# Kernel tuning notes

Measured on AMD Instinct MI355X. Metric: run time of the kernel, lower is better.

## Reference

```python
import jax, jax.numpy as jnp
import numpy as np
import math

RES = 1024
HEADS = 16
HEAD_RES = RES // HEADS
B, S = 2, 2048


def setup_inputs() -> dict:
    key = jax.random.key(0)
    kx, kq, kk, kv = jax.random.split(key, 4)
    scale = 1.0 / math.sqrt(RES)
    return {
        "x": jax.random.normal(kx, (B, S, RES), dtype=jnp.float32),
        "Wq": jax.random.normal(kq, (RES, RES), dtype=jnp.float32) * scale,
        "Wk": jax.random.normal(kk, (RES, RES), dtype=jnp.float32) * scale,
        "Wv": jax.random.normal(kv, (RES, RES), dtype=jnp.float32) * scale,
    }


def reference(x, Wq, Wk, Wv):
    batch, seq, _ = x.shape
    # projections (torch Linear without bias: x @ W.T; here W stored as [in, out])
    def split_heads(t):
        return t.reshape(batch, seq, HEADS, HEAD_RES).transpose(0, 2, 1, 3)  # [B,H,S,D]
    q = split_heads(x @ Wq)
    k = split_heads(x @ Wk)
    v = split_heads(x @ Wv)
    scores = jnp.einsum("bhsd,bhtd->bhst", q, k) / math.sqrt(HEAD_RES)
    attn = jax.nn.softmax(scores, axis=-1)
    out = jnp.einsum("bhst,bhtd->bhsd", attn, v)  # [B,H,S,D]
    return out.transpose(0, 2, 1, 3).reshape(batch, seq, RES)
```

## Files before the change

### kernel.cpp

```cpp
#include <hip/hip_runtime.h>

typedef _Float16 f16;
typedef _Float16 half8 __attribute__((ext_vector_type(8)));
typedef float f32x4 __attribute__((ext_vector_type(4)));
typedef unsigned int u32x4 __attribute__((ext_vector_type(4)));

#define RES 1024
#define NH 16
#define HD 64
#define BATCH 2
#define SEQ 2048
#define M_ROWS (BATCH * SEQ)

__device__ __forceinline__ void gload_lds16(const void* g, void* l) {
  __builtin_amdgcn_global_load_lds(
      (const __attribute__((address_space(1))) unsigned int*)g,
      (__attribute__((address_space(3))) unsigned int*)l, 16, 0, 0);
}

__device__ __forceinline__ unsigned pk16(float a, float b) {
  auto h = __builtin_amdgcn_cvt_pkrtz(a, b);
  return __builtin_bit_cast(unsigned, h);
}

__device__ __forceinline__ unsigned pk16_rne(float a, float b) {
  unsigned short la = __builtin_bit_cast(unsigned short, (f16)a);
  unsigned short hb = __builtin_bit_cast(unsigned short, (f16)b);
  return (unsigned)la | ((unsigned)hb << 16);
}

__device__ __forceinline__ void swap32(unsigned a, unsigned b, unsigned& x, unsigned& y) {
#if __has_builtin(__builtin_amdgcn_permlane32_swap)
  auto t = __builtin_amdgcn_permlane32_swap(a, b, false, false);
  x = (unsigned)t[0];
  y = (unsigned)t[1];
#else
  unsigned ax = __shfl_xor(a, 32), bx = __shfl_xor(b, 32);
  int hi = (threadIdx.x & 63) >> 5;
  x = hi ? bx : a;
  y = hi ? b : ax;
#endif
}

__device__ __forceinline__ void swap16(unsigned a, unsigned b, unsigned& x, unsigned& y) {
#if __has_builtin(__builtin_amdgcn_permlane16_swap)
  auto t = __builtin_amdgcn_permlane16_swap(a, b, false, false);
  x = (unsigned)t[0];
  y = (unsigned)t[1];
#else
  unsigned ax = __shfl_xor(a, 16), bx = __shfl_xor(b, 16);
  int q1 = ((threadIdx.x & 63) >> 4) & 1;
  x = q1 ? bx : a;
  y = q1 ? b : ax;
#endif
}

__global__ __launch_bounds__(256) void prep_kernel(const float* __restrict__ x,
                                                   const float* __restrict__ Wq,
                                                   const float* __restrict__ Wk,
                                                   const float* __restrict__ Wv,
                                                   f16* __restrict__ xh,
                                                   f16* __restrict__ Wt) {
  __shared__ float tile[32][33];
  int bid = blockIdx.x;
  int tid = threadIdx.x;
  if (bid < 2048) {
    int idx = bid * 256 + tid;
    const float4* xv = (const float4*)x;
    float4 a = xv[idx * 2];
    float4 b = xv[idx * 2 + 1];
    half8 h;
    h[0] = (f16)a.x; h[1] = (f16)a.y; h[2] = (f16)a.z; h[3] = (f16)a.w;
    h[4] = (f16)b.x; h[5] = (f16)b.y; h[6] = (f16)b.z; h[7] = (f16)b.w;
    ((half8*)xh)[idx] = h;
  } else {
    int wb = bid - 2048;
    int bz = wb >> 10;
    int rem = wb & 1023;
    int by = rem >> 5, bx = rem & 31;
    const float* W = bz == 0 ? Wq : (bz == 1 ? Wk : Wv);
    f16* Wo = Wt + (size_t)bz * RES * RES;
    int tx = tid & 31, ty = tid >> 5;
#pragma unroll
    for (int i = 0; i < 4; i++)
      tile[ty + i * 8][tx] = W[(size_t)(by * 32 + ty + i * 8) * RES + bx * 32 + tx];
    __syncthreads();
#pragma unroll
    for (int i = 0; i < 4; i++)
      Wo[(size_t)(bx * 32 + ty + i * 8) * RES + by * 32 + tx] = (f16)tile[tx][ty + i * 8];
  }
}

__global__ __launch_bounds__(256) void proj_gemm_kernel(const f16* __restrict__ xh,
                                                        const f16* __restrict__ Wt,
                                                        f16* __restrict__ Qh,
                                                        f16* __restrict__ Kh,
                                                        f16* __restrict__ Vt) {
  int proj = blockIdx.z;
  const f16* Bt = Wt + (size_t)proj * RES * RES;
  int m0 = blockIdx.x * 128;
  int n0 = blockIdx.y * 128;
  __shared__ alignas(16) f16 Als[128 * 32];
  __shared__ alignas(16) f16 Bls[128 * 32];
  int t = threadIdx.x, lane = t & 63, w = t >> 6;
  int l15 = lane & 15, quad = lane >> 4;
  int wm = w >> 1, wn = w & 1;

  f32x4 zero = {0.f, 0.f, 0.f, 0.f};
  f32x4 acc[4][4];
#pragma unroll
  for (int mt = 0; mt < 4; mt++)
#pragma unroll
    for (int nt = 0; nt < 4; nt++) acc[mt][nt] = zero;

  for (int k0 = 0; k0 < RES; k0 += 32) {
#pragma unroll
    for (int i = 0; i < 2; i++) {
      int wl = i * 256 + w * 64;
      int linear = wl + lane;
      int row = linear >> 2;
      int kk = (linear & 3) * 8;
      gload_lds16(xh + (size_t)(m0 + row) * RES + k0 + kk, &Als[wl * 8]);
      gload_lds16(Bt + (size_t)(n0 + row) * RES + k0 + kk, &Bls[wl * 8]);
    }
    __syncthreads();
    half8 af[4], bf[4];
#pragma unroll
    for (int mt = 0; mt < 4; mt++)
      af[mt] = *(const half8*)&Als[(wm * 64 + mt * 16 + l15) * 32 + quad * 8];
#pragma unroll
    for (int nt = 0; nt < 4; nt++)
      bf[nt] = *(const half8*)&Bls[(wn * 64 + nt * 16 + l15) * 32 + quad * 8];
#pragma unroll
    for (int mt = 0; mt < 4; mt++)
#pragma unroll
      for (int nt = 0; nt < 4; nt++)
        acc[mt][nt] = __builtin_amdgcn_mfma_f32_16x16x32_f16(af[mt], bf[nt], acc[mt][nt], 0, 0, 0);
    __syncthreads();
  }

  if (proj == 2) {
    int rowb = m0 + wm * 64;
    int b = rowb >> 11;
    int sbase = rowb & (SEQ - 1);
    int h = (n0 + wn * 64) >> 6;
    size_t bh = (size_t)b * NH + h;
#pragma unroll
    for (int nt = 0; nt < 4; nt++) {
      unsigned wp[4][2];
#pragma unroll
      for (int mt = 0; mt < 4; mt++) {
        wp[mt][0] = pk16_rne(acc[mt][nt][0], acc[mt][nt][1]);
        wp[mt][1] = pk16_rne(acc[mt][nt][2], acc[mt][nt][3]);
      }
#pragma unroll
      for (int ks = 0; ks < 2; ks++) {
        u32x4 pw;
#pragma unroll
        for (int i = 0; i < 2; i++) {
          unsigned a, bb, xx, yy;
          swap32(wp[2 * ks][i], wp[2 * ks + 1][i], a, bb);
          swap16(a, bb, xx, yy);
          pw[i] = xx;
          pw[2 + i] = yy;
        }
        int d = nt * 16 + l15;
        int s0 = sbase + ks * 32 + quad * 8;
        *(half8*)&Vt[(bh * HD + d) * SEQ + s0] = __builtin_bit_cast(half8, pw);
      }
    }
  } else {
#pragma unroll
    for (int mt = 0; mt < 4; mt++) {
#pragma unroll
      for (int nt = 0; nt < 4; nt++) {
#pragma unroll
        for (int r = 0; r < 4; r++) {
          int row = m0 + wm * 64 + mt * 16 + quad * 4 + r;
          int col = n0 + wn * 64 + nt * 16 + l15;
          f16 v = (f16)acc[mt][nt][r];
          int b = row >> 11, s = row & (SEQ - 1);
          int h = col >> 6, d = col & (HD - 1);
          size_t bh = (size_t)b * NH + h;
          if (proj == 0)
            Qh[(bh * SEQ + s) * HD + d] = v;
          else
            Kh[(bh * SEQ + s) * HD + d] = v;
        }
      }
    }
  }
}

__global__ __launch_bounds__(128, 3) void flash_kernel(const f16* __restrict__ Qh,
                                                       const f16* __restrict__ Kh,
                                                       const f16* __restrict__ Vt,
                                                       float* __restrict__ out) {
  int L = blockIdx.x;
  int xcd = L & 7, slot = L >> 3;
  int bh = ((slot >> 5) << 3) | xcd;
  int qt = slot & 31;
  int b = bh >> 4, h = bh & 15;
  int tid = threadIdx.x;
  int lane = tid & 63, w = tid >> 6;
  int l15 = lane & 15, quad = lane >> 4;
  int qrow0 = qt * 64 + w * 32;

  __shared__ alignas(16) f16 Kls[64 * 64];
  __shared__ alignas(16) f16 Vls[64 * 64];

  const f16* kbase = Kh + (size_t)bh * SEQ * HD;
  const f16* vbase = Vt + (size_t)bh * HD * SEQ;

  int srow = tid >> 3;
  int schunk = tid & 7;

  const f16* qptr = Qh + ((size_t)bh * SEQ + qrow0 + l15) * HD + quad * 8;
  half8 qf[2][2];
  qf[0][0] = *(const half8*)qptr;
  qf[0][1] = *(const half8*)(qptr + 32);
  qf[1][0] = *(const half8*)(qptr + 16 * HD);
  qf[1][1] = *(const half8*)(qptr + 16 * HD + 32);
#pragma unroll
  for (int q2 = 0; q2 < 2; q2++)
#pragma unroll
    for (int ks = 0; ks < 2; ks++)
#pragma unroll
      for (int j = 0; j < 8; j++) qf[q2][ks][j] *= (f16)0.125f;

  f32x4 zero = {0.f, 0.f, 0.f, 0.f};
  float l_acc[2] = {0.f, 0.f};
  f32x4 o[2][4];
#pragma unroll
  for (int q2 = 0; q2 < 2; q2++)
#pragma unroll
    for (int nt = 0; nt < 4; nt++) o[q2][nt] = zero;

  int swz0 = (quad ^ (l15 & 7)) * 8;
  int swz1 = ((quad + 4) ^ (l15 & 7)) * 8;

  auto stage = [&](int kv0) {
#pragma unroll
    for (int rd = 0; rd < 4; rd++) {
      int row = rd * 16 + srow;
      int pc = schunk ^ (row & 7);
      gload_lds16(kbase + ((size_t)(kv0 + row) << 6) + pc * 8,
                  &Kls[rd * 1024 + w * 512]);
      gload_lds16(vbase + ((size_t)row * SEQ) + kv0 + pc * 8,
                  &Vls[rd * 1024 + w * 512]);
    }
  };

  stage(0);

  for (int kv0 = 0; kv0 < SEQ; kv0 += 64) {
    __syncthreads();

    half8 kf0[4], kf1[4];
#pragma unroll
    for (int tt = 0; tt < 4; tt++) {
      int row = tt * 16 + l15;
      kf0[tt] = *(const half8*)&Kls[row * 64 + swz0];
      kf1[tt] = *(const half8*)&Kls[row * 64 + swz1];
    }

    half8 pa[2][2];
#pragma unroll
    for (int q2 = 0; q2 < 2; q2++) {
      f32x4 sc[4];
#pragma unroll
      for (int tt = 0; tt < 4; tt++) {
        sc[tt] = __builtin_amdgcn_mfma_f32_16x16x32_f16(kf0[tt], qf[q2][0], zero, 0, 0, 0);
        sc[tt] = __builtin_amdgcn_mfma_f32_16x16x32_f16(kf1[tt], qf[q2][1], sc[tt], 0, 0, 0);
      }
      float ps = 0.f;
#pragma unroll
      for (int tt = 0; tt < 4; tt++)
#pragma unroll
        for (int r = 0; r < 4; r++) { sc[tt][r] = __expf(sc[tt][r]); ps += sc[tt][r]; }
      ps += __shfl_xor(ps, 16);
      ps += __shfl_xor(ps, 32);
      l_acc[q2] += ps;

      unsigned wp[4][2];
#pragma unroll
      for (int tt = 0; tt < 4; tt++) {
        wp[tt][0] = pk16(sc[tt][0], sc[tt][1]);
        wp[tt][1] = pk16(sc[tt][2], sc[tt][3]);
      }
#pragma unroll
      for (int ks = 0; ks < 2; ks++) {
        u32x4 pw;
#pragma unroll
        for (int i = 0; i < 2; i++) {
          unsigned a, bb, x, y;
          swap32(wp[2 * ks][i], wp[2 * ks + 1][i], a, bb);
          swap16(a, bb, x, y);
          pw[i] = x;
          pw[2 + i] = y;
        }
        pa[q2][ks] = __builtin_bit_cast(half8, pw);
      }
    }

    half8 vf0[4], vf1[4];
#pragma unroll
    for (int nt = 0; nt < 4; nt++) {
      int row = nt * 16 + l15;
      vf0[nt] = *(const half8*)&Vls[row * 64 + swz0];
      vf1[nt] = *(const half8*)&Vls[row * 64 + swz1];
    }

    __syncthreads();

    if (kv0 + 64 < SEQ) stage(kv0 + 64);

#pragma unroll
    for (int q2 = 0; q2 < 2; q2++)
#pragma unroll
      for (int ks = 0; ks < 2; ks++)
#pragma unroll
        for (int nt = 0; nt < 4; nt++)
          o[q2][nt] = __builtin_amdgcn_mfma_f32_16x16x32_f16(pa[q2][ks], ks ? vf1[nt] : vf0[nt], o[q2][nt], 0, 0, 0);
  }

#pragma unroll
  for (int q2 = 0; q2 < 2; q2++) {
    float linv[4];
#pragma unroll
    for (int r = 0; r < 4; r++) linv[r] = 1.0f / __shfl(l_acc[q2], quad * 4 + r);
#pragma unroll
    for (int nt = 0; nt < 4; nt++) {
#pragma unroll
      for (int r = 0; r < 4; r++) {
        int s = qrow0 + q2 * 16 + quad * 4 + r;
        out[((size_t)b * SEQ + s) * RES + h * HD + nt * 16 + l15] = o[q2][nt][r] * linv[r];
      }
    }
  }
}

extern "C" void kernel_launch(void* const* d_in, const int* in_sizes, int n_in,
                              void* d_out, int out_size, void* d_ws, size_t ws_size,
                              hipStream_t stream) {
  (void)in_sizes; (void)n_in; (void)out_size; (void)ws_size;
  const float* x  = (const float*)d_in[0];
  const float* Wq = (const float*)d_in[1];
  const float* Wk = (const float*)d_in[2];
  const float* Wv = (const float*)d_in[3];
  float* out = (float*)d_out;

  f16* xh = (f16*)d_ws;
  f16* Wt = xh + (size_t)M_ROWS * RES;
  f16* Qh = Wt + (size_t)3 * RES * RES;
  f16* Kh = Qh + (size_t)BATCH * NH * SEQ * HD;
  f16* Vt = Kh + (size_t)BATCH * NH * SEQ * HD;

  prep_kernel<<<2048 + 3072, 256, 0, stream>>>(x, Wq, Wk, Wv, xh, Wt);
  proj_gemm_kernel<<<dim3(M_ROWS / 128, RES / 128, 3), 256, 0, stream>>>(xh, Wt, Qh, Kh, Vt);
  flash_kernel<<<1024, 128, 0, stream>>>(Qh, Kh, Vt, out);
}
```

Before: 167.1 us.

## Enlarge projection GEMM tiles to 256x256 with double-buffered swizzled LDS

The QKV projection GEMM now uses 256x256 output tiles with 512 threads, 8x4 MFMA accumulator tiles per wave, and K-steps of 64. LDS is double buffered so the next K slice is fetched with global_load_lds while the current one is computed, using vmcnt waits and raw s_barrier. An XOR swizzle on the LDS layout is meant to cut bank conflicts. The aim is more data reuse per load and overlap of memory with compute. In exchange the grid shrinks to 192 blocks, fewer than the CU count, and register and LDS pressure rise (128 KB of LDS).

```diff
diff --git a/kernel.cpp b/kernel.cpp
--- a/kernel.cpp
+++ b/kernel.cpp
@@ -91,97 +91,125 @@
   }
 }
 
-__global__ __launch_bounds__(256) void proj_gemm_kernel(const f16* __restrict__ xh,
+__global__ __launch_bounds__(512) void proj_gemm_kernel(const f16* __restrict__ xh,
                                                         const f16* __restrict__ Wt,
                                                         f16* __restrict__ Qh,
                                                         f16* __restrict__ Kh,
                                                         f16* __restrict__ Vt) {
   int proj = blockIdx.z;
   const f16* Bt = Wt + (size_t)proj * RES * RES;
-  int m0 = blockIdx.x * 128;
-  int n0 = blockIdx.y * 128;
-  __shared__ alignas(16) f16 Als[128 * 32];
-  __shared__ alignas(16) f16 Bls[128 * 32];
-  int t = threadIdx.x, lane = t & 63, w = t >> 6;
+  int m0 = blockIdx.x * 256;
+  int n0 = blockIdx.y * 256;
+  __shared__ alignas(16) f16 Als[2][256 * 64];
+  __shared__ alignas(16) f16 Bls[2][256 * 64];
+  int tid = threadIdx.x, lane = tid & 63, w = tid >> 6;
   int l15 = lane & 15, quad = lane >> 4;
-  int wm = w >> 1, wn = w & 1;
+  int wr = w >> 2, wc = w & 3;
 
   f32x4 zero = {0.f, 0.f, 0.f, 0.f};
-  f32x4 acc[4][4];
-#pragma unroll
-  for (int mt = 0; mt < 4; mt++)
+  f32x4 acc[8][4];
+#pragma unroll
+  for (int mt = 0; mt < 8; mt++)
 #pragma unroll
     for (int nt = 0; nt < 4; nt++) acc[mt][nt] = zero;
 
-  for (int k0 = 0; k0 < RES; k0 += 32) {
-#pragma unroll
-    for (int i = 0; i < 2; i++) {
-      int wl = i * 256 + w * 64;
-      int linear = wl + lane;
-      int row = linear >> 2;
-      int kk = (linear & 3) * 8;
-      gload_lds16(xh + (size_t)(m0 + row) * RES + k0 + kk, &Als[wl * 8]);
-      gload_lds16(Bt + (size_t)(n0 + row) * RES + k0 + kk, &Bls[wl * 8]);
-    }
-    __syncthreads();
-    half8 af[4], bf[4];
-#pragma unroll
-    for (int mt = 0; mt < 4; mt++)
-      af[mt] = *(const half8*)&Als[(wm * 64 + mt * 16 + l15) * 32 + quad * 8];
-#pragma unroll
-    for (int nt = 0; nt < 4; nt++)
-      bf[nt] = *(const half8*)&Bls[(wn * 64 + nt * 16 + l15) * 32 + quad * 8];
-#pragma unroll
-    for (int mt = 0; mt < 4; mt++)
-#pragma unroll
-      for (int nt = 0; nt < 4; nt++)
-        acc[mt][nt] = __builtin_amdgcn_mfma_f32_16x16x32_f16(af[mt], bf[nt], acc[mt][nt], 0, 0, 0);
-    __syncthreads();
-  }
+  auto stageAB = [&](int k0, int pb) {
+#pragma unroll
+    for (int rnd = 0; rnd < 4; rnd++) {
+      int row = rnd * 64 + (tid >> 3);
+      int pc = (tid & 7) ^ (row & 7);
+      gload_lds16(xh + (size_t)(m0 + row) * RES + k0 + pc * 8,
+                  &Als[pb][rnd * 4096 + w * 512]);
+      gload_lds16(Bt + (size_t)(n0 + row) * RES + k0 + pc * 8,
+                  &Bls[pb][rnd * 4096 + w * 512]);
+    }
+  };
+
+  constexpr int KSTEPS = RES / 64;
+  stageAB(0, 0);
+
+  for (int it = 0; it < KSTEPS; ++it) {
+    int pb = it & 1;
+    if (it + 1 < KSTEPS) {
+      stageAB((it + 1) * 64, pb ^ 1);
+      asm volatile("s_waitcnt vmcnt(8)" ::: "memory");
+    } else {
+      asm volatile("s_waitcnt vmcnt(0)" ::: "memory");
+    }
+    __builtin_amdgcn_sched_barrier(0);
+    __builtin_amdgcn_s_barrier();
+    __builtin_amdgcn_sched_barrier(0);
+
+#pragma unroll
+    for (int half = 0; half < 2; half++) {
+      half8 af[8], bf[4];
+#pragma unroll
+      for (int mt = 0; mt < 8; mt++) {
+        int arow = wr * 128 + mt * 16 + l15;
+        af[mt] = *(const half8*)&Als[pb][arow * 64 + ((half * 4 + quad) ^ (arow & 7)) * 8];
+      }
+#pragma unroll
+      for (int nt = 0; nt < 4; nt++) {
+        int brow = wc * 64 + nt * 16 + l15;
+        bf[nt] = *(const half8*)&Bls[pb][brow * 64 + ((half * 4 + quad) ^ (brow & 7)) * 8];
+      }
+#pragma unroll
+      for (int mt = 0; mt < 8; mt++)
+#pragma unroll
+        for (int nt = 0; nt < 4; nt++)
+          acc[mt][nt] = __builtin_amdgcn_mfma_f32_16x16x32_f16(af[mt], bf[nt], acc[mt][nt], 0, 0, 0);
+    }
+
+    __builtin_amdgcn_sched_barrier(0);
+    __builtin_amdgcn_s_barrier();
+    __builtin_amdgcn_sched_barrier(0);
+  }
+
+  int rowbase = m0 + wr * 128;
+  int b = rowbase >> 11;
+  int sbase = rowbase & (SEQ - 1);
+  int colbase = n0 + wc * 64;
+  int h = colbase >> 6;
+  size_t bh = (size_t)b * NH + h;
 
   if (proj == 2) {
-    int rowb = m0 + wm * 64;
-    int b = rowb >> 11;
-    int sbase = rowb & (SEQ - 1);
-    int h = (n0 + wn * 64) >> 6;
-    size_t bh = (size_t)b * NH + h;
 #pragma unroll
     for (int nt = 0; nt < 4; nt++) {
-      unsigned wp[4][2];
-#pragma unroll
-      for (int mt = 0; mt < 4; mt++) {
-        wp[mt][0] = pk16_rne(acc[mt][nt][0], acc[mt][nt][1]);
-        wp[mt][1] = pk16_rne(acc[mt][nt][2], acc[mt][nt][3]);
-      }
-#pragma unroll
-      for (int ks = 0; ks < 2; ks++) {
-        u32x4 pw;
-#pragma unroll
-        for (int i = 0; i < 2; i++) {
-          unsigned a, bb, xx, yy;
-          swap32(wp[2 * ks][i], wp[2 * ks + 1][i], a, bb);
-          swap16(a, bb, xx, yy);
-          pw[i] = xx;
-          pw[2 + i] = yy;
+      int d = nt * 16 + l15;
+#pragma unroll
+      for (int g = 0; g < 2; g++) {
+        unsigned wp[4][2];
+#pragma unroll
+        for (int mtl = 0; mtl < 4; mtl++) {
+          wp[mtl][0] = pk16_rne(acc[g * 4 + mtl][nt][0], acc[g * 4 + mtl][nt][1]);
+          wp[mtl][1] = pk16_rne(acc[g * 4 + mtl][nt][2], acc[g * 4 + mtl][nt][3]);
         }
-        int d = nt * 16 + l15;
-        int s0 = sbase + ks * 32 + quad * 8;
-        *(half8*)&Vt[(bh * HD + d) * SEQ + s0] = __builtin_bit_cast(half8, pw);
+#pragma unroll
+        for (int ks = 0; ks < 2; ks++) {
+          u32x4 pw;
+#pragma unroll
+          for (int i = 0; i < 2; i++) {
+            unsigned a, bb2, xx, yy;
+            swap32(wp[2 * ks][i], wp[2 * ks + 1][i], a, bb2);
+            swap16(a, bb2, xx, yy);
+            pw[i] = xx;
+            pw[2 + i] = yy;
+          }
+          int s0 = sbase + g * 64 + ks * 32 + quad * 8;
+          *(half8*)&Vt[(bh * HD + d) * SEQ + s0] = __builtin_bit_cast(half8, pw);
+        }
       }
     }
   } else {
 #pragma unroll
-    for (int mt = 0; mt < 4; mt++) {
+    for (int mt = 0; mt < 8; mt++) {
 #pragma unroll
       for (int nt = 0; nt < 4; nt++) {
 #pragma unroll
         for (int r = 0; r < 4; r++) {
-          int row = m0 + wm * 64 + mt * 16 + quad * 4 + r;
-          int col = n0 + wn * 64 + nt * 16 + l15;
+          int s = sbase + mt * 16 + quad * 4 + r;
+          int d = nt * 16 + l15;
           f16 v = (f16)acc[mt][nt][r];
-          int b = row >> 11, s = row & (SEQ - 1);
-          int h = col >> 6, d = col & (HD - 1);
-          size_t bh = (size_t)b * NH + h;
           if (proj == 0)
             Qh[(bh * SEQ + s) * HD + d] = v;
           else
@@ -357,6 +385,6 @@
   f16* Vt = Kh + (size_t)BATCH * NH * SEQ * HD;
 
   prep_kernel<<<2048 + 3072, 256, 0, stream>>>(x, Wq, Wk, Wv, xh, Wt);
-  proj_gemm_kernel<<<dim3(M_ROWS / 128, RES / 128, 3), 256, 0, stream>>>(xh, Wt, Qh, Kh, Vt);
+  proj_gemm_kernel<<<dim3(M_ROWS / 256, RES / 256, 3), 512, 0, stream>>>(xh, Wt, Qh, Kh, Vt);
   flash_kernel<<<1024, 128, 0, stream>>>(Qh, Kh, Vt, out);
 }
```

New measurement: 173.2 us. 3.6% more time.
